# Kernel optimization log

Measured on AMD Instinct MI355X. Metric: run time of the kernel, lower is better.

The kernel has to match this reference:

```python
import jax, jax.numpy as jnp
import numpy as np

EPS = 1e-5  # torch LayerNorm default
H, DH = 8, 64  # heads, dim_head


def _ln(x, g, b):
    mu = jnp.mean(x, axis=-1, keepdims=True)
    var = jnp.var(x, axis=-1, keepdims=True)
    return (x - mu) / jnp.sqrt(var + EPS) * g + b


def setup_inputs() -> dict:
    key = jax.random.key(0)
    ks = jax.random.split(key, 8)
    B, N, M, D, CD = 4, 2048, 256, 1024, 768
    J = M + 1 + N  # context + null + self
    return {
        "x": jax.random.normal(ks[0], (B, N, D), jnp.float32),
        "context": jax.random.normal(ks[1], (B, M, CD), jnp.float32),
        "att_bias": jax.random.normal(ks[2], (B, H, N, J), jnp.float32) * 0.02,
        "ln_g": jnp.ones((D,), jnp.float32),
        "ln_b": jnp.zeros((D,), jnp.float32),
        "null_kv": jax.random.normal(ks[3], (2, DH), jnp.float32),
        "Wq": jax.random.normal(ks[4], (D, H * DH), jnp.float32) * 0.02,
        "Wkv": jax.random.normal(ks[5], (D, 2 * DH), jnp.float32) * 0.02,
        "cln_g": jnp.ones((CD,), jnp.float32),
        "cln_b": jnp.zeros((CD,), jnp.float32),
        "Wc": jax.random.normal(ks[6], (CD, 2 * DH), jnp.float32) * 0.02,
        "bc": jnp.zeros((2 * DH,), jnp.float32),
        "Wo": jax.random.normal(ks[7], (H * DH, D), jnp.float32) * 0.02,
        "oln_g": jnp.ones((D,), jnp.float32),
        "oln_b": jnp.zeros((D,), jnp.float32),
    }


def reference(x, context, att_bias, ln_g, ln_b, null_kv, Wq, Wkv,
              cln_g, cln_b, Wc, bc, Wo, oln_g, oln_b):
    B, N, D = x.shape
    scale = DH ** -0.5
    xn = _ln(x, ln_g, ln_b)
    # queries: per-head [b,h,n,dh], pre-scaled
    q = (xn @ Wq).reshape(B, N, H, DH).transpose(0, 2, 1, 3) * scale
    # shared single-head k/v [b,n,dh]
    kv = xn @ Wkv
    k, v = kv[..., :DH], kv[..., DH:]
    # context k/v [b,m,dh]
    ckv = _ln(context, cln_g, cln_b) @ Wc + bc
    ck, cv = ckv[..., :DH], ckv[..., DH:]
    # null kv token [b,1,dh]
    nk = jnp.broadcast_to(null_kv[0], (B, 1, DH))
    nv = jnp.broadcast_to(null_kv[1], (B, 1, DH))
    # torch order: cat null first, then context -> (ck, nk, k)
    k = jnp.concatenate([ck, nk, k], axis=1)  # [b, j, dh]
    v = jnp.concatenate([cv, nv, v], axis=1)
    score = jnp.einsum('bhid,bjd->bhij', q, k) + att_bias
    probs = jax.nn.softmax(score.astype(jnp.float32), axis=-1).astype(v.dtype)
    att = jnp.einsum('bhij,bjd->bhid', probs, v)
    att = att.transpose(0, 2, 1, 3).reshape(B, N, H * DH)
    return _ln(att @ Wo, oln_g, oln_b)
```

## Files before the change

### kernel.cpp

```cpp
#include <hip/hip_runtime.h>
#include <hip/hip_bf16.h>
#include <cstdint>
#include <cstddef>

#define Bq  4
#define Nq  2048
#define Mq  256
#define Dq  1024
#define CDq 768
#define Hq  8
#define DHq 64
#define Jq  2305
#define QKVN 640
#define NCH 37
#define J2  (NCH * 64)

typedef __bf16  bf16x8 __attribute__((ext_vector_type(8)));
typedef float   f32x4  __attribute__((ext_vector_type(4)));
typedef float   f32x4u __attribute__((ext_vector_type(4), aligned(4)));
typedef float   f32x16 __attribute__((ext_vector_type(16)));
typedef short   s16x8  __attribute__((ext_vector_type(8)));
typedef unsigned int u32x4 __attribute__((ext_vector_type(4)));
typedef unsigned short u16;
typedef unsigned int   u32;

__device__ __forceinline__ u16 f2b(float v) {
  unsigned x = __builtin_bit_cast(unsigned, v);
  unsigned r = (x + 0x7fffu + ((x >> 16) & 1u)) >> 16;
  return (u16)r;
}
__device__ __forceinline__ float b2f(u16 u) {
  unsigned x = ((unsigned)u) << 16;
  return __builtin_bit_cast(float, x);
}
__device__ __forceinline__ u32 cvtpk(float lo, float hi) {
  u32 r;
  asm("v_cvt_pk_bf16_f32 %0, %1, %2" : "=v"(r) : "v"(lo), "v"(hi));
  return r;
}
__device__ __forceinline__ void pswap(u32& a, u32& b) {
  asm volatile("v_permlane32_swap_b32 %0, %1" : "+v"(a), "+v"(b));
}
__device__ __forceinline__ f32x4 mfma16(bf16x8 a, bf16x8 b, f32x4 c) {
  return __builtin_amdgcn_mfma_f32_16x16x32_bf16(a, b, c, 0, 0, 0);
}
__device__ __forceinline__ f32x16 mfma32(bf16x8 a, bf16x8 b, f32x16 c) {
  return __builtin_amdgcn_mfma_f32_32x32x16_bf16(a, b, c, 0, 0, 0);
}
__device__ __forceinline__ bf16x8 frag_ld(const u16* p) {
  return __builtin_bit_cast(bf16x8, *(const s16x8*)p);
}
__device__ __forceinline__ void stout(float* p, float v) { *p = v; }
__device__ __forceinline__ void stout(u16*   p, float v) { *p = f2b(v); }

__device__ __forceinline__ void gl_lds16(const void* gSrc, void* ldsDst) {
  __builtin_amdgcn_global_load_lds(
      (const __attribute__((address_space(1))) void*)gSrc,
      (__attribute__((address_space(3))) void*)ldsDst, 16, 0, 0);
}

__global__ __launch_bounds__(256) void prep_kernel(
    const float* __restrict__ x,   const float* __restrict__ ln_g,
    const float* __restrict__ ln_b, u16* __restrict__ xn,
    const float* __restrict__ ctx, const float* __restrict__ cln_g,
    const float* __restrict__ cln_b, u16* __restrict__ ctxn,
    const float* __restrict__ Wq, const float* __restrict__ Wkv,
    const float* __restrict__ Wc, const float* __restrict__ Wo,
    u16* __restrict__ WqkvT, u16* __restrict__ WcT, u16* __restrict__ WoT) {
  const int tid = threadIdx.x;
  if (blockIdx.x < Bq * Nq + Bq * Mq) {
    const int row = blockIdx.x;
    const float* in; const float* g; const float* bb; u16* out; int D;
    if (row < Bq * Nq) {
      in = x + (size_t)row * Dq; g = ln_g; bb = ln_b;
      out = xn + (size_t)row * Dq; D = Dq;
    } else {
      int r2 = row - Bq * Nq;
      in = ctx + (size_t)r2 * CDq; g = cln_g; bb = cln_b;
      out = ctxn + (size_t)r2 * CDq; D = CDq;
    }
    __shared__ float buf[1024];
    __shared__ float red[8];
    float s = 0.f, s2 = 0.f;
    for (int i = tid; i < D; i += 256) {
      float v = in[i];
      buf[i] = v;
      s += v; s2 += v * v;
    }
    #pragma unroll
    for (int off = 32; off; off >>= 1) {
      s  += __shfl_down(s,  off);
      s2 += __shfl_down(s2, off);
    }
    if ((tid & 63) == 0) { red[tid >> 6] = s; red[4 + (tid >> 6)] = s2; }
    __syncthreads();
    float sum = red[0] + red[1] + red[2] + red[3];
    float sq  = red[4] + red[5] + red[6] + red[7];
    float mean = sum / D;
    float var  = sq / D - mean * mean;
    float rstd = rsqrtf(var + 1e-5f);
    for (int i = tid; i < D; i += 256)
      out[i] = f2b((buf[i] - mean) * rstd * g[i] + bb[i]);
  } else {
    __shared__ float T[32][33];
    int bid = blockIdx.x - (Bq * Nq + Bq * Mq);
    const float* W; u16* WT; int K, N, bx, by;
    if (bid < 512)      { W = Wq;  WT = WqkvT;                    K = 1024; N = 512;  bx = bid % 16;        by = bid / 16; }
    else if (bid < 640) { W = Wkv; WT = WqkvT + (size_t)512*1024; K = 1024; N = 128;  bx = (bid-512) % 4;   by = (bid-512) / 4; }
    else if (bid < 736) { W = Wc;  WT = WcT;                      K = 768;  N = 128;  bx = (bid-640) % 4;   by = (bid-640) / 4; }
    else                { W = Wo;  WT = WoT;                      K = 512;  N = 1024; bx = (bid-736) % 32;  by = (bid-736) / 32; }
    const int n0 = bx * 32, k0 = by * 32;
    const int tx = tid & 31, ty = tid >> 5;
    #pragma unroll
    for (int i = 0; i < 32; i += 8)
      T[ty + i][tx] = W[(size_t)(k0 + ty + i) * N + n0 + tx];
    __syncthreads();
    #pragma unroll
    for (int i = 0; i < 32; i += 8)
      WT[(size_t)(n0 + ty + i) * K + k0 + tx] = f2b(T[tx][ty + i]);
  }
}

__global__ __launch_bounds__(256) void ln_out_kernel(
    const float* __restrict__ in, const float* __restrict__ g,
    const float* __restrict__ bb, float* __restrict__ out) {
  const int row = blockIdx.x;
  const int tid = threadIdx.x;
  __shared__ float buf[1024];
  __shared__ float red[8];
  const float* xr = in + (size_t)row * Dq;
  float s = 0.f, s2 = 0.f;
  for (int i = tid; i < Dq; i += 256) {
    float v = xr[i];
    buf[i] = v;
    s += v; s2 += v * v;
  }
  #pragma unroll
  for (int off = 32; off; off >>= 1) {
    s  += __shfl_down(s,  off);
    s2 += __shfl_down(s2, off);
  }
  if ((tid & 63) == 0) { red[tid >> 6] = s; red[4 + (tid >> 6)] = s2; }
  __syncthreads();
  float sum = red[0] + red[1] + red[2] + red[3];
  float sq  = red[4] + red[5] + red[6] + red[7];
  float mean = sum / Dq;
  float var  = sq / Dq - mean * mean;
  float rstd = rsqrtf(var + 1e-5f);
  for (int i = tid; i < Dq; i += 256)
    out[(size_t)row * Dq + i] = (buf[i] - mean) * rstd * g[i] + bb[i];
}

template <typename OT>
__device__ __forceinline__ void gemm_body(const u16* __restrict__ A,
                                          const u16* __restrict__ BT,
                                          OT* __restrict__ C,
                                          int N, int K, int m0, int n0,
                                          u16* Al, u16* Bl) {
  const int tid  = threadIdx.x;
  const int lane = tid & 63, wave = tid >> 6;
  const int l16  = lane & 15, lhi = lane >> 4;
  const int wm = (wave >> 1) * 64, wn = (wave & 1) * 64;

  const int offB = (wave << 10) + (lane << 4);
  const int srow = offB >> 6;
  const int scby = offB & 63;

  f32x4 acc[4][4];
  #pragma unroll
  for (int i = 0; i < 4; ++i)
    #pragma unroll
    for (int j = 0; j < 4; ++j) acc[i][j] = f32x4{0.f, 0.f, 0.f, 0.f};

  for (int k0 = 0; k0 < K; k0 += 32) {
    __syncthreads();
    #pragma unroll
    for (int c = 0; c < 2; ++c) {
      gl_lds16((const char*)(A  + (size_t)(m0 + srow + c * 64) * K + k0) + scby,
               (char*)Al + c * 4096 + (wave << 10));
      gl_lds16((const char*)(BT + (size_t)(n0 + srow + c * 64) * K + k0) + scby,
               (char*)Bl + c * 4096 + (wave << 10));
    }
    __syncthreads();

    bf16x8 af[4], bfr[4];
    #pragma unroll
    for (int mt = 0; mt < 4; ++mt)
      af[mt] = frag_ld(Al + (wm + mt * 16 + l16) * 32 + lhi * 8);
    #pragma unroll
    for (int nt = 0; nt < 4; ++nt)
      bfr[nt] = frag_ld(Bl + (wn + nt * 16 + l16) * 32 + lhi * 8);
    __builtin_amdgcn_s_setprio(1);
    #pragma unroll
    for (int mt = 0; mt < 4; ++mt)
      #pragma unroll
      for (int nt = 0; nt < 4; ++nt)
        acc[mt][nt] = mfma16(af[mt], bfr[nt], acc[mt][nt]);
    __builtin_amdgcn_s_setprio(0);
  }

  #pragma unroll
  for (int mt = 0; mt < 4; ++mt)
    #pragma unroll
    for (int nt = 0; nt < 4; ++nt)
      #pragma unroll
      for (int r = 0; r < 4; ++r)
        stout(C + (size_t)(m0 + wm + mt * 16 + lhi * 4 + r) * N
                + (n0 + wn + nt * 16 + l16),
              acc[mt][nt][r]);
}

__global__ __launch_bounds__(256) void gemm_qkv_ckv(
    const u16* __restrict__ xn, const u16* __restrict__ WqkvT,
    u16* __restrict__ qkv,
    const u16* __restrict__ ctxn, const u16* __restrict__ WcT,
    u16* __restrict__ ckvb) {
  const u16 *A, *BT; u16* C; int N, K, m0, n0;
  if (blockIdx.y < 5) {
    A = xn; BT = WqkvT; C = qkv; N = QKVN; K = Dq;
    m0 = blockIdx.x * 128; n0 = blockIdx.y * 128;
  } else {
    if (blockIdx.x >= 8) return;
    A = ctxn; BT = WcT; C = ckvb; N = 2 * DHq; K = CDq;
    m0 = blockIdx.x * 128; n0 = 0;
  }
  __shared__ __align__(16) u16 Al[128 * 32];
  __shared__ __align__(16) u16 Bl[128 * 32];
  gemm_body<u16>(A, BT, C, N, K, m0, n0, Al, Bl);
}

__global__ __launch_bounds__(256) void gemm128f(const u16* __restrict__ A,
                                                const u16* __restrict__ BT,
                                                float* __restrict__ C,
                                                int N, int K) {
  __shared__ __align__(16) u16 Al[128 * 32];
  __shared__ __align__(16) u16 Bl[128 * 32];
  gemm_body<float>(A, BT, C, N, K, blockIdx.x * 128, blockIdx.y * 128, Al, Bl);
}

__global__ void build_kv(const u16* __restrict__ qkv,
                         const u16* __restrict__ ckvb,
                         const float* __restrict__ nullkv,
                         const float* __restrict__ bc,
                         u16* __restrict__ Kt, u16* __restrict__ Vt) {
  int idx = blockIdx.x * 256 + threadIdx.x;
  if (idx >= Bq * J2 * 64) return;
  int d = idx & 63;
  int t = idx >> 6;
  int j = t % J2;
  int b = t / J2;
  float k = 0.f, v = 0.f;
  if (j < Mq) {
    const u16* p = ckvb + (size_t)(b * Mq + j) * 128;
    k = b2f(p[d])      + bc[d];
    v = b2f(p[64 + d]) + bc[64 + d];
  } else if (j == Mq) {
    k = nullkv[d];
    v = nullkv[64 + d];
  } else if (j < Jq) {
    const u16* p = qkv + (size_t)(b * Nq + (j - Mq - 1)) * QKVN + 512;
    k = b2f(p[d]);
    v = b2f(p[64 + d]);
  }
  int ch = j >> 6, row = j & 63;
  char* tbase = (char*)Kt + ((size_t)(b * NCH + ch)) * 8192;
  *(u16*)(tbase + row * 128 + ((d << 1) ^ ((row & 7) << 4))) = f2b(k);
  char* vbase = (char*)Vt + ((size_t)(b * NCH + ch)) * 8192;
  *(u16*)(vbase + d * 128 + ((row << 1) ^ ((d & 7) << 4))) = f2b(v);
}

__global__ __launch_bounds__(128) void attn_kernel(
    const u16* __restrict__ qkv, const u16* __restrict__ Kt,
    const u16* __restrict__ Vt, const float* __restrict__ bias,
    u16* __restrict__ att) {
  __shared__ __align__(16) u16 Kl [2][4096];
  __shared__ __align__(16) u16 VTl[2][4096];
  const int tid  = threadIdx.x;
  const int wave = tid >> 6, lane = tid & 63;
  const int l = lane & 31, hi = lane >> 5;
  const int qt = blockIdx.x, h = blockIdx.y, b = blockIdx.z;
  const int qrow0 = qt * 64 + wave * 32;

  bf16x8 qf[4];
  {
    const u16* qp = qkv + ((size_t)(b * Nq + qrow0 + l)) * QKVN
                        + h * DHq + hi * 8;
    #pragma unroll
    for (int kt = 0; kt < 4; ++kt) qf[kt] = frag_ld(qp + kt * 16);
  }

  float m_s = -INFINITY, l_s = 0.f;
  f32x16 oacc[2];
  #pragma unroll
  for (int dt = 0; dt < 2; ++dt)
    #pragma unroll
    for (int r = 0; r < 16; ++r) oacc[dt][r] = 0.f;

  const float* bp = bias
      + ((size_t)((b * Hq + h) * (size_t)Nq + qrow0 + l)) * Jq + 4 * hi;

  const size_t tb0 = (size_t)b * NCH;
  const int soff = (wave << 12) + (lane << 4);

  auto stage = [&](int buf, int ch) {
    const char* kt_ = (const char*)Kt + (tb0 + ch) * 8192 + soff;
    const char* vt_ = (const char*)Vt + (tb0 + ch) * 8192 + soff;
    char* kl = (char*)&Kl[buf][0]  + (wave << 12);
    char* vl = (char*)&VTl[buf][0] + (wave << 12);
    #pragma unroll
    for (int i = 0; i < 4; ++i) {
      gl_lds16(kt_ + i * 1024, kl + i * 1024);
      gl_lds16(vt_ + i * 1024, vl + i * 1024);
    }
  };

  f32x4 bv[2][4];
  auto loadBias = [&](int ch) {
    const int jc = ch * 64;
    if (ch < NCH - 1) {
      #pragma unroll
      for (int jt = 0; jt < 2; ++jt)
        #pragma unroll
        for (int g = 0; g < 4; ++g)
          bv[jt][g] = (f32x4)(*(const f32x4u*)(bp + jc + jt * 32 + 8 * g));
    } else {
      #pragma unroll
      for (int jt = 0; jt < 2; ++jt)
        #pragma unroll
        for (int g = 0; g < 4; ++g)
          #pragma unroll
          for (int e = 0; e < 4; ++e) {
            int jg = jc + jt * 32 + 8 * g + 4 * hi + e;
            bv[jt][g][e] = (jg < Jq) ? bp[jc + jt * 32 + 8 * g + e] : -1e30f;
          }
    }
  };

  stage(0, 0);
  loadBias(0);
  __syncthreads();

  for (int ch = 0; ch < NCH; ++ch) {
    const int cur = ch & 1;
    if (ch + 1 < NCH) stage(cur ^ 1, ch + 1);
    const char* kbase = (const char*)&Kl[cur][0];
    const char* vbase = (const char*)&VTl[cur][0];

    f32x16 sacc[2];
    #pragma unroll
    for (int jt = 0; jt < 2; ++jt)
      #pragma unroll
      for (int r = 0; r < 16; ++r) sacc[jt][r] = 0.f;
    __builtin_amdgcn_s_setprio(1);
    #pragma unroll
    for (int jt = 0; jt < 2; ++jt) {
      const int row = jt * 32 + l;
      const int sw = (row & 7) << 4;
      #pragma unroll
      for (int kt = 0; kt < 4; ++kt) {
        bf16x8 kf = frag_ld((const u16*)(kbase + row * 128
                                         + ((kt * 32 + hi * 16) ^ sw)));
        sacc[jt] = mfma32(kf, qf[kt], sacc[jt]);
      }
    }
    __builtin_amdgcn_s_setprio(0);

    float sv[2][16];
    #pragma unroll
    for (int jt = 0; jt < 2; ++jt)
      #pragma unroll
      for (int r = 0; r < 16; ++r)
        sv[jt][r] = sacc[jt][r] * 0.125f + bv[jt][r >> 2][r & 3];
    if (ch + 1 < NCH) loadBias(ch + 1);

    float pmax = sv[0][0];
    #pragma unroll
    for (int jt = 0; jt < 2; ++jt)
      #pragma unroll
      for (int r = 0; r < 16; ++r) pmax = fmaxf(pmax, sv[jt][r]);
    pmax = fmaxf(pmax, __shfl_xor(pmax, 32));

    if (__any(pmax > m_s + 8.f)) {
      float mnew = fmaxf(m_s, pmax);
      float corr = __expf(m_s - mnew);
      l_s *= corr;
      m_s = mnew;
      #pragma unroll
      for (int r = 0; r < 16; ++r) {
        float c = __shfl(corr, (r & 3) + 8 * (r >> 2) + 4 * hi);
        oacc[0][r] *= c;
        oacc[1][r] *= c;
      }
    }

    float ps = 0.f;
    #pragma unroll
    for (int jt = 0; jt < 2; ++jt)
      #pragma unroll
      for (int r = 0; r < 16; ++r) {
        float pv = __expf(sv[jt][r] - m_s);
        sv[jt][r] = pv;
        ps += pv;
      }
    ps += __shfl_xor(ps, 32);
    l_s += ps;

    u32 pk[2][8];
    #pragma unroll
    for (int jt = 0; jt < 2; ++jt)
      #pragma unroll
      for (int g = 0; g < 4; ++g) {
        pk[jt][2 * g]     = cvtpk(sv[jt][4 * g],     sv[jt][4 * g + 1]);
        pk[jt][2 * g + 1] = cvtpk(sv[jt][4 * g + 2], sv[jt][4 * g + 3]);
      }

    #pragma unroll
    for (int kt = 0; kt < 4; ++kt) {
      const int t = kt & 1, js = kt >> 1;
      u32 a0 = pk[js][4 * t],     b0 = pk[js][4 * t + 2];
      u32 a1 = pk[js][4 * t + 1], b1 = pk[js][4 * t + 3];
      pswap(a0, b0);
      pswap(a1, b1);
      bf16x8 paf = __builtin_bit_cast(bf16x8, u32x4{a0, a1, b0, b1});
      __builtin_amdgcn_s_setprio(1);
      #pragma unroll
      for (int dt = 0; dt < 2; ++dt) {
        const int vrow = dt * 32 + l;
        bf16x8 vf = frag_ld((const u16*)(vbase + vrow * 128
                     + ((kt * 32 + hi * 16) ^ ((vrow & 7) << 4))));
        oacc[dt] = mfma32(paf, vf, oacc[dt]);
      }
      __builtin_amdgcn_s_setprio(0);
    }
    __syncthreads();
  }

  float linv = 1.0f / l_s;
  #pragma unroll
  for (int r = 0; r < 16; ++r) {
    const int qo = (r & 3) + 8 * (r >> 2) + 4 * hi;
    float inv = __shfl(linv, qo);
    u16* op = att + ((size_t)(b * Nq + qrow0 + qo)) * (Hq * DHq) + h * DHq + l;
    op[0]  = f2b(oacc[0][r] * inv);
    op[32] = f2b(oacc[1][r] * inv);
  }
}

extern "C" void kernel_launch(void* const* d_in, const int* in_sizes, int n_in,
                              void* d_out, int out_size, void* d_ws, size_t ws_size,
                              hipStream_t stream) {
  const float* x       = (const float*)d_in[0];
  const float* context = (const float*)d_in[1];
  const float* att_bias= (const float*)d_in[2];
  const float* ln_g    = (const float*)d_in[3];
  const float* ln_b    = (const float*)d_in[4];
  const float* null_kv = (const float*)d_in[5];
  const float* Wq      = (const float*)d_in[6];
  const float* Wkv     = (const float*)d_in[7];
  const float* cln_g   = (const float*)d_in[8];
  const float* cln_b   = (const float*)d_in[9];
  const float* Wc      = (const float*)d_in[10];
  const float* bc      = (const float*)d_in[11];
  const float* Wo      = (const float*)d_in[12];
  const float* oln_g   = (const float*)d_in[13];
  const float* oln_b   = (const float*)d_in[14];
  float* out = (float*)d_out;

  char* p = (char*)d_ws;
  auto alloc = [&](size_t bytes) {
    void* r = (void*)p;
    p += (bytes + 255) & ~(size_t)255;
    return r;
  };
  u16* xn     = (u16*)alloc((size_t)Bq * Nq * Dq * 2);
  u16* ctxn   = (u16*)alloc((size_t)Bq * Mq * CDq * 2);
  u16* WqkvT  = (u16*)alloc((size_t)QKVN * Dq * 2);
  u16* WcT    = (u16*)alloc((size_t)2 * DHq * CDq * 2);
  u16* WoT    = (u16*)alloc((size_t)Dq * Hq * DHq * 2);
  u16* qkv    = (u16*)alloc((size_t)Bq * Nq * QKVN * 2);
  u16* ckvb   = (u16*)alloc((size_t)Bq * Mq * 2 * DHq * 2);
  u16* Ktil   = (u16*)alloc((size_t)Bq * NCH * 8192);
  u16* Vtil   = (u16*)alloc((size_t)Bq * NCH * 8192);
  u16* attb   = (u16*)alloc((size_t)Bq * Nq * Hq * DHq * 2);
  float* y    = (float*)alloc((size_t)Bq * Nq * Dq * 4);

  prep_kernel<<<Bq * Nq + Bq * Mq + 1248, 256, 0, stream>>>(
      x, ln_g, ln_b, xn, context, cln_g, cln_b, ctxn,
      Wq, Wkv, Wc, Wo, WqkvT, WcT, WoT);

  gemm_qkv_ckv<<<dim3(Bq * Nq / 128, 6), 256, 0, stream>>>(
      xn, WqkvT, qkv, ctxn, WcT, ckvb);

  build_kv<<<(Bq * J2 * 64 + 255) / 256, 256, 0, stream>>>(
      qkv, ckvb, null_kv, bc, Ktil, Vtil);

  attn_kernel<<<dim3(Nq / 64, Hq, Bq), 128, 0, stream>>>(
      qkv, Ktil, Vtil, att_bias, attb);

  gemm128f<<<dim3(Bq * Nq / 128, Dq / 128), 256, 0, stream>>>(
      attb, WoT, y, Dq, Hq * DHq);
  ln_out_kernel<<<Bq * Nq, 256, 0, stream>>>(y, oln_g, oln_b, out);
}
```

Before: 261.7 us.

## Load K/V fragments directly from global memory, dropping LDS staging

The attention kernel no longer stages K and V chunks into double-buffered shared memory. Each wave now loads its MFMA fragments straight from global (L2-cached) memory into registers, and the XOR swizzle is removed from the repack kernel. Bias prefetch is reorganised into ping-pong register buffers with an unrolled two-step loop. This removes the LDS traffic and the per-chunk __syncthreads, but both waves of a block now fetch the same K/V data from global memory, which adds cache traffic and register pressure.

```diff
diff --git a/kernel.cpp b/kernel.cpp
--- a/kernel.cpp
+++ b/kernel.cpp
@@ -17,7 +17,6 @@
 
 typedef __bf16  bf16x8 __attribute__((ext_vector_type(8)));
 typedef float   f32x4  __attribute__((ext_vector_type(4)));
-typedef float   f32x4u __attribute__((ext_vector_type(4), aligned(4)));
 typedef float   f32x16 __attribute__((ext_vector_type(16)));
 typedef short   s16x8  __attribute__((ext_vector_type(8)));
 typedef unsigned int u32x4 __attribute__((ext_vector_type(4)));
@@ -264,17 +263,15 @@
   }
   int ch = j >> 6, row = j & 63;
   char* tbase = (char*)Kt + ((size_t)(b * NCH + ch)) * 8192;
-  *(u16*)(tbase + row * 128 + ((d << 1) ^ ((row & 7) << 4))) = f2b(k);
+  *(u16*)(tbase + row * 128 + (d << 1)) = f2b(k);
   char* vbase = (char*)Vt + ((size_t)(b * NCH + ch)) * 8192;
-  *(u16*)(vbase + d * 128 + ((row << 1) ^ ((d & 7) << 4))) = f2b(v);
+  *(u16*)(vbase + d * 128 + (row << 1)) = f2b(v);
 }
 
 __global__ __launch_bounds__(128) void attn_kernel(
     const u16* __restrict__ qkv, const u16* __restrict__ Kt,
     const u16* __restrict__ Vt, const float* __restrict__ bias,
     u16* __restrict__ att) {
-  __shared__ __align__(16) u16 Kl [2][4096];
-  __shared__ __align__(16) u16 VTl[2][4096];
   const int tid  = threadIdx.x;
   const int wave = tid >> 6, lane = tid & 63;
   const int l = lane & 31, hi = lane >> 5;
@@ -299,30 +296,17 @@
   const float* bp = bias
       + ((size_t)((b * Hq + h) * (size_t)Nq + qrow0 + l)) * Jq + 4 * hi;
 
-  const size_t tb0 = (size_t)b * NCH;
-  const int soff = (wave << 12) + (lane << 4);
-
-  auto stage = [&](int buf, int ch) {
-    const char* kt_ = (const char*)Kt + (tb0 + ch) * 8192 + soff;
-    const char* vt_ = (const char*)Vt + (tb0 + ch) * 8192 + soff;
-    char* kl = (char*)&Kl[buf][0]  + (wave << 12);
-    char* vl = (char*)&VTl[buf][0] + (wave << 12);
-    #pragma unroll
-    for (int i = 0; i < 4; ++i) {
-      gl_lds16(kt_ + i * 1024, kl + i * 1024);
-      gl_lds16(vt_ + i * 1024, vl + i * 1024);
-    }
-  };
-
-  f32x4 bv[2][4];
-  auto loadBias = [&](int ch) {
+  const char* kb0 = (const char*)Kt + (size_t)b * NCH * 8192 + l * 128 + hi * 16;
+  const char* vb0 = (const char*)Vt + (size_t)b * NCH * 8192 + l * 128 + hi * 16;
+
+  auto loadBias = [&](f32x4 (&bv)[2][4], int ch) {
     const int jc = ch * 64;
     if (ch < NCH - 1) {
       #pragma unroll
       for (int jt = 0; jt < 2; ++jt)
         #pragma unroll
         for (int g = 0; g < 4; ++g)
-          bv[jt][g] = (f32x4)(*(const f32x4u*)(bp + jc + jt * 32 + 8 * g));
+          bv[jt][g] = *(const f32x4*)(bp + jc + jt * 32 + 8 * g);
     } else {
       #pragma unroll
       for (int jt = 0; jt < 2; ++jt)
@@ -336,15 +320,25 @@
     }
   };
 
-  stage(0, 0);
-  loadBias(0);
-  __syncthreads();
-
-  for (int ch = 0; ch < NCH; ++ch) {
-    const int cur = ch & 1;
-    if (ch + 1 < NCH) stage(cur ^ 1, ch + 1);
-    const char* kbase = (const char*)&Kl[cur][0];
-    const char* vbase = (const char*)&VTl[cur][0];
+  f32x4 bvA[2][4], bvB[2][4];
+  loadBias(bvA, 0);
+
+  auto body = [&](int ch, f32x4 (&bvC)[2][4], f32x4 (&bvN)[2][4]) {
+    const char* kc = kb0 + (size_t)ch * 8192;
+    const char* vc = vb0 + (size_t)ch * 8192;
+
+    bf16x8 kf[8], vf[8];
+    #pragma unroll
+    for (int jt = 0; jt < 2; ++jt)
+      #pragma unroll
+      for (int kt = 0; kt < 4; ++kt)
+        kf[jt * 4 + kt] = frag_ld((const u16*)(kc + jt * 4096 + kt * 32));
+    #pragma unroll
+    for (int dt = 0; dt < 2; ++dt)
+      #pragma unroll
+      for (int kt = 0; kt < 4; ++kt)
+        vf[dt * 4 + kt] = frag_ld((const u16*)(vc + dt * 4096 + kt * 32));
+    if (ch + 1 < NCH) loadBias(bvN, ch + 1);
 
     f32x16 sacc[2];
     #pragma unroll
@@ -353,16 +347,10 @@
       for (int r = 0; r < 16; ++r) sacc[jt][r] = 0.f;
     __builtin_amdgcn_s_setprio(1);
     #pragma unroll
-    for (int jt = 0; jt < 2; ++jt) {
-      const int row = jt * 32 + l;
-      const int sw = (row & 7) << 4;
-      #pragma unroll
-      for (int kt = 0; kt < 4; ++kt) {
-        bf16x8 kf = frag_ld((const u16*)(kbase + row * 128
-                                         + ((kt * 32 + hi * 16) ^ sw)));
-        sacc[jt] = mfma32(kf, qf[kt], sacc[jt]);
-      }
-    }
+    for (int jt = 0; jt < 2; ++jt)
+      #pragma unroll
+      for (int kt = 0; kt < 4; ++kt)
+        sacc[jt] = mfma32(kf[jt * 4 + kt], qf[kt], sacc[jt]);
     __builtin_amdgcn_s_setprio(0);
 
     float sv[2][16];
@@ -370,8 +358,7 @@
     for (int jt = 0; jt < 2; ++jt)
       #pragma unroll
       for (int r = 0; r < 16; ++r)
-        sv[jt][r] = sacc[jt][r] * 0.125f + bv[jt][r >> 2][r & 3];
-    if (ch + 1 < NCH) loadBias(ch + 1);
+        sv[jt][r] = sacc[jt][r] * 0.125f + bvC[jt][r >> 2][r & 3];
 
     float pmax = sv[0][0];
     #pragma unroll
@@ -424,15 +411,18 @@
       bf16x8 paf = __builtin_bit_cast(bf16x8, u32x4{a0, a1, b0, b1});
       __builtin_amdgcn_s_setprio(1);
       #pragma unroll
-      for (int dt = 0; dt < 2; ++dt) {
-        const int vrow = dt * 32 + l;
-        bf16x8 vf = frag_ld((const u16*)(vbase + vrow * 128
-                     + ((kt * 32 + hi * 16) ^ ((vrow & 7) << 4))));
-        oacc[dt] = mfma32(paf, vf, oacc[dt]);
-      }
+      for (int dt = 0; dt < 2; ++dt)
+        oacc[dt] = mfma32(paf, vf[dt * 4 + kt], oacc[dt]);
       __builtin_amdgcn_s_setprio(0);
     }
-    __syncthreads();
+  };
+
+  int ch = 0;
+  while (true) {
+    body(ch, bvA, bvB);
+    if (++ch == NCH) break;
+    body(ch, bvB, bvA);
+    if (++ch == NCH) break;
   }
 
   float linv = 1.0f / l_s;
```

New measurement: 316.7 us. 1.21x slower.

## Prefetch attention bias two chunks ahead and store output GEMM in bf16

Applied to the files above, without the earlier changes.

The attention loop is unrolled four ways and rotates four bias register sets, so bias loads for chunks ch+2 and ch+3 are issued early. Barriers use partial vmcnt waits so outstanding bias loads can stay in flight across chunks, which targets the latency of the large att_bias stream. Separately, the output projection now writes bf16 instead of fp32, and the final LayerNorm reads bf16 with vector loads, halving the intermediate's traffic at some precision cost. The extra bias registers may raise register pressure in the attention kernel.

```diff
diff --git a/kernel.cpp b/kernel.cpp
--- a/kernel.cpp
+++ b/kernel.cpp
@@ -20,6 +20,7 @@
 typedef float   f32x4u __attribute__((ext_vector_type(4), aligned(4)));
 typedef float   f32x16 __attribute__((ext_vector_type(16)));
 typedef short   s16x8  __attribute__((ext_vector_type(8)));
+typedef short   s16x4  __attribute__((ext_vector_type(4)));
 typedef unsigned int u32x4 __attribute__((ext_vector_type(4)));
 typedef unsigned short u16;
 typedef unsigned int   u32;
@@ -122,18 +123,22 @@
 }
 
 __global__ __launch_bounds__(256) void ln_out_kernel(
-    const float* __restrict__ in, const float* __restrict__ g,
+    const u16* __restrict__ in, const float* __restrict__ g,
     const float* __restrict__ bb, float* __restrict__ out) {
   const int row = blockIdx.x;
   const int tid = threadIdx.x;
   __shared__ float buf[1024];
   __shared__ float red[8];
-  const float* xr = in + (size_t)row * Dq;
+  const u16* xr = in + (size_t)row * Dq;
   float s = 0.f, s2 = 0.f;
-  for (int i = tid; i < Dq; i += 256) {
-    float v = xr[i];
-    buf[i] = v;
-    s += v; s2 += v * v;
+  {
+    s16x4 v4 = *(const s16x4*)(xr + tid * 4);
+    #pragma unroll
+    for (int e = 0; e < 4; ++e) {
+      float v = b2f((u16)v4[e]);
+      buf[tid * 4 + e] = v;
+      s += v; s2 += v * v;
+    }
   }
   #pragma unroll
   for (int off = 32; off; off >>= 1) {
@@ -147,8 +152,11 @@
   float mean = sum / Dq;
   float var  = sq / Dq - mean * mean;
   float rstd = rsqrtf(var + 1e-5f);
-  for (int i = tid; i < Dq; i += 256)
+  #pragma unroll
+  for (int e = 0; e < 4; ++e) {
+    int i = tid * 4 + e;
     out[(size_t)row * Dq + i] = (buf[i] - mean) * rstd * g[i] + bb[i];
+  }
 }
 
 template <typename OT>
@@ -229,13 +237,13 @@
   gemm_body<u16>(A, BT, C, N, K, m0, n0, Al, Bl);
 }
 
-__global__ __launch_bounds__(256) void gemm128f(const u16* __restrict__ A,
+__global__ __launch_bounds__(256) void gemm128b(const u16* __restrict__ A,
                                                 const u16* __restrict__ BT,
-                                                float* __restrict__ C,
+                                                u16* __restrict__ C,
                                                 int N, int K) {
   __shared__ __align__(16) u16 Al[128 * 32];
   __shared__ __align__(16) u16 Bl[128 * 32];
-  gemm_body<float>(A, BT, C, N, K, blockIdx.x * 128, blockIdx.y * 128, Al, Bl);
+  gemm_body<u16>(A, BT, C, N, K, blockIdx.x * 128, blockIdx.y * 128, Al, Bl);
 }
 
 __global__ void build_kv(const u16* __restrict__ qkv,
@@ -314,8 +322,7 @@
     }
   };
 
-  f32x4 bv[2][4];
-  auto loadBias = [&](int ch) {
+  auto loadBias = [&](f32x4 (&bv)[2][4], int ch) {
     const int jc = ch * 64;
     if (ch < NCH - 1) {
       #pragma unroll
@@ -336,13 +343,8 @@
     }
   };
 
-  stage(0, 0);
-  loadBias(0);
-  __syncthreads();
-
-  for (int ch = 0; ch < NCH; ++ch) {
+  auto compute = [&](int ch, f32x4 (&bvC)[2][4]) {
     const int cur = ch & 1;
-    if (ch + 1 < NCH) stage(cur ^ 1, ch + 1);
     const char* kbase = (const char*)&Kl[cur][0];
     const char* vbase = (const char*)&VTl[cur][0];
 
@@ -365,19 +367,17 @@
     }
     __builtin_amdgcn_s_setprio(0);
 
-    float sv[2][16];
     #pragma unroll
     for (int jt = 0; jt < 2; ++jt)
       #pragma unroll
       for (int r = 0; r < 16; ++r)
-        sv[jt][r] = sacc[jt][r] * 0.125f + bv[jt][r >> 2][r & 3];
-    if (ch + 1 < NCH) loadBias(ch + 1);
-
-    float pmax = sv[0][0];
+        sacc[jt][r] = sacc[jt][r] * 0.125f + bvC[jt][r >> 2][r & 3];
+
+    float pmax = sacc[0][0];
     #pragma unroll
     for (int jt = 0; jt < 2; ++jt)
       #pragma unroll
-      for (int r = 0; r < 16; ++r) pmax = fmaxf(pmax, sv[jt][r]);
+      for (int r = 0; r < 16; ++r) pmax = fmaxf(pmax, sacc[jt][r]);
     pmax = fmaxf(pmax, __shfl_xor(pmax, 32));
 
     if (__any(pmax > m_s + 8.f)) {
@@ -398,8 +398,8 @@
     for (int jt = 0; jt < 2; ++jt)
       #pragma unroll
       for (int r = 0; r < 16; ++r) {
-        float pv = __expf(sv[jt][r] - m_s);
-        sv[jt][r] = pv;
+        float pv = __expf(sacc[jt][r] - m_s);
+        sacc[jt][r] = pv;
         ps += pv;
       }
     ps += __shfl_xor(ps, 32);
@@ -410,8 +410,8 @@
     for (int jt = 0; jt < 2; ++jt)
       #pragma unroll
       for (int g = 0; g < 4; ++g) {
-        pk[jt][2 * g]     = cvtpk(sv[jt][4 * g],     sv[jt][4 * g + 1]);
-        pk[jt][2 * g + 1] = cvtpk(sv[jt][4 * g + 2], sv[jt][4 * g + 3]);
+        pk[jt][2 * g]     = cvtpk(sacc[jt][4 * g],     sacc[jt][4 * g + 1]);
+        pk[jt][2 * g + 1] = cvtpk(sacc[jt][4 * g + 2], sacc[jt][4 * g + 3]);
       }
 
     #pragma unroll
@@ -432,7 +432,57 @@
       }
       __builtin_amdgcn_s_setprio(0);
     }
-    __syncthreads();
+  };
+
+  auto barKeep = [&]() {
+    asm volatile("s_waitcnt vmcnt(16)" ::: "memory");
+    __builtin_amdgcn_s_barrier();
+    __builtin_amdgcn_sched_barrier(0);
+  };
+  auto barDrain = [&]() {
+    asm volatile("s_waitcnt vmcnt(0)" ::: "memory");
+    __builtin_amdgcn_s_barrier();
+    __builtin_amdgcn_sched_barrier(0);
+  };
+
+  f32x4 bv0[2][4], bv1[2][4], bv2[2][4], bv3[2][4];
+  stage(0, 0);
+  loadBias(bv0, 0);
+  loadBias(bv1, 1);
+  barKeep();
+
+  int ch = 0;
+  while (true) {
+    {
+      if (ch + 1 < NCH) stage((ch & 1) ^ 1, ch + 1);
+      const bool full = (ch + 3 < NCH);
+      if (ch + 2 < NCH) loadBias(bv2, ch + 2);
+      if (ch + 3 < NCH) loadBias(bv3, ch + 3);
+      compute(ch, bv0);
+      if (ch + 1 < NCH) { if (full) barKeep(); else barDrain(); }
+    }
+    if (++ch == NCH) break;
+    {
+      if (ch + 1 < NCH) stage((ch & 1) ^ 1, ch + 1);
+      compute(ch, bv1);
+      if (ch + 1 < NCH) barDrain();
+    }
+    if (++ch == NCH) break;
+    {
+      if (ch + 1 < NCH) stage((ch & 1) ^ 1, ch + 1);
+      const bool full = (ch + 3 < NCH);
+      if (ch + 2 < NCH) loadBias(bv0, ch + 2);
+      if (ch + 3 < NCH) loadBias(bv1, ch + 3);
+      compute(ch, bv2);
+      if (ch + 1 < NCH) { if (full) barKeep(); else barDrain(); }
+    }
+    if (++ch == NCH) break;
+    {
+      if (ch + 1 < NCH) stage((ch & 1) ^ 1, ch + 1);
+      compute(ch, bv3);
+      if (ch + 1 < NCH) barDrain();
+    }
+    if (++ch == NCH) break;
   }
 
   float linv = 1.0f / l_s;
@@ -482,7 +532,7 @@
   u16* Ktil   = (u16*)alloc((size_t)Bq * NCH * 8192);
   u16* Vtil   = (u16*)alloc((size_t)Bq * NCH * 8192);
   u16* attb   = (u16*)alloc((size_t)Bq * Nq * Hq * DHq * 2);
-  float* y    = (float*)alloc((size_t)Bq * Nq * Dq * 4);
+  u16* y      = (u16*)alloc((size_t)Bq * Nq * Dq * 2);
 
   prep_kernel<<<Bq * Nq + Bq * Mq + 1248, 256, 0, stream>>>(
       x, ln_g, ln_b, xn, context, cln_g, cln_b, ctxn,
@@ -497,7 +547,7 @@
   attn_kernel<<<dim3(Nq / 64, Hq, Bq), 128, 0, stream>>>(
       qkv, Ktil, Vtil, att_bias, attb);
 
-  gemm128f<<<dim3(Bq * Nq / 128, Dq / 128), 256, 0, stream>>>(
+  gemm128b<<<dim3(Bq * Nq / 128, Dq / 128), 256, 0, stream>>>(
       attb, WoT, y, Dq, Hq * DHq);
   ln_out_kernel<<<Bq * Nq, 256, 0, stream>>>(y, oln_g, oln_b, out);
 }
```

After: 275.4 us. 1.05x slower.

## Give each attention wave private K/V buffers and store out-proj result as bf16

Applied to the files above, without the earlier changes.

The attention kernel now gives each wave its own double-buffered copy of the K/V tiles. This removes the block-wide __syncthreads per chunk and replaces it with an explicit vmcnt wait, with bias prefetch ping-ponged between two register sets. Shared memory doubles and every wave loads the full tile redundantly. Separately, the output projection GEMM now writes bf16 instead of fp32, and the final LayerNorm reads bf16 vectors. This halves that intermediate's traffic at a small precision cost before normalization.

```diff
diff --git a/kernel.cpp b/kernel.cpp
--- a/kernel.cpp
+++ b/kernel.cpp
@@ -20,6 +20,7 @@
 typedef float   f32x4u __attribute__((ext_vector_type(4), aligned(4)));
 typedef float   f32x16 __attribute__((ext_vector_type(16)));
 typedef short   s16x8  __attribute__((ext_vector_type(8)));
+typedef short   s16x4  __attribute__((ext_vector_type(4)));
 typedef unsigned int u32x4 __attribute__((ext_vector_type(4)));
 typedef unsigned short u16;
 typedef unsigned int   u32;
@@ -122,18 +123,22 @@
 }
 
 __global__ __launch_bounds__(256) void ln_out_kernel(
-    const float* __restrict__ in, const float* __restrict__ g,
+    const u16* __restrict__ in, const float* __restrict__ g,
     const float* __restrict__ bb, float* __restrict__ out) {
   const int row = blockIdx.x;
   const int tid = threadIdx.x;
   __shared__ float buf[1024];
   __shared__ float red[8];
-  const float* xr = in + (size_t)row * Dq;
+  const u16* xr = in + (size_t)row * Dq;
   float s = 0.f, s2 = 0.f;
-  for (int i = tid; i < Dq; i += 256) {
-    float v = xr[i];
-    buf[i] = v;
-    s += v; s2 += v * v;
+  {
+    s16x4 v4 = *(const s16x4*)(xr + tid * 4);
+    #pragma unroll
+    for (int e = 0; e < 4; ++e) {
+      float v = b2f((u16)v4[e]);
+      buf[tid * 4 + e] = v;
+      s += v; s2 += v * v;
+    }
   }
   #pragma unroll
   for (int off = 32; off; off >>= 1) {
@@ -147,8 +152,11 @@
   float mean = sum / Dq;
   float var  = sq / Dq - mean * mean;
   float rstd = rsqrtf(var + 1e-5f);
-  for (int i = tid; i < Dq; i += 256)
+  #pragma unroll
+  for (int e = 0; e < 4; ++e) {
+    int i = tid * 4 + e;
     out[(size_t)row * Dq + i] = (buf[i] - mean) * rstd * g[i] + bb[i];
+  }
 }
 
 template <typename OT>
@@ -229,13 +237,13 @@
   gemm_body<u16>(A, BT, C, N, K, m0, n0, Al, Bl);
 }
 
-__global__ __launch_bounds__(256) void gemm128f(const u16* __restrict__ A,
+__global__ __launch_bounds__(256) void gemm128b(const u16* __restrict__ A,
                                                 const u16* __restrict__ BT,
-                                                float* __restrict__ C,
+                                                u16* __restrict__ C,
                                                 int N, int K) {
   __shared__ __align__(16) u16 Al[128 * 32];
   __shared__ __align__(16) u16 Bl[128 * 32];
-  gemm_body<float>(A, BT, C, N, K, blockIdx.x * 128, blockIdx.y * 128, Al, Bl);
+  gemm_body<u16>(A, BT, C, N, K, blockIdx.x * 128, blockIdx.y * 128, Al, Bl);
 }
 
 __global__ void build_kv(const u16* __restrict__ qkv,
@@ -273,8 +281,8 @@
     const u16* __restrict__ qkv, const u16* __restrict__ Kt,
     const u16* __restrict__ Vt, const float* __restrict__ bias,
     u16* __restrict__ att) {
-  __shared__ __align__(16) u16 Kl [2][4096];
-  __shared__ __align__(16) u16 VTl[2][4096];
+  __shared__ __align__(16) u16 Kl [2][2][4096];
+  __shared__ __align__(16) u16 VTl[2][2][4096];
   const int tid  = threadIdx.x;
   const int wave = tid >> 6, lane = tid & 63;
   const int l = lane & 31, hi = lane >> 5;
@@ -300,22 +308,21 @@
       + ((size_t)((b * Hq + h) * (size_t)Nq + qrow0 + l)) * Jq + 4 * hi;
 
   const size_t tb0 = (size_t)b * NCH;
-  const int soff = (wave << 12) + (lane << 4);
+  const int soff = lane << 4;
 
   auto stage = [&](int buf, int ch) {
     const char* kt_ = (const char*)Kt + (tb0 + ch) * 8192 + soff;
     const char* vt_ = (const char*)Vt + (tb0 + ch) * 8192 + soff;
-    char* kl = (char*)&Kl[buf][0]  + (wave << 12);
-    char* vl = (char*)&VTl[buf][0] + (wave << 12);
-    #pragma unroll
-    for (int i = 0; i < 4; ++i) {
+    char* kl = (char*)&Kl[wave][buf][0];
+    char* vl = (char*)&VTl[wave][buf][0];
+    #pragma unroll
+    for (int i = 0; i < 8; ++i) {
       gl_lds16(kt_ + i * 1024, kl + i * 1024);
       gl_lds16(vt_ + i * 1024, vl + i * 1024);
     }
   };
 
-  f32x4 bv[2][4];
-  auto loadBias = [&](int ch) {
+  auto loadBias = [&](f32x4 (&bv)[2][4], int ch) {
     const int jc = ch * 64;
     if (ch < NCH - 1) {
       #pragma unroll
@@ -336,15 +343,23 @@
     }
   };
 
+  f32x4 bvA[2][4], bvB[2][4];
   stage(0, 0);
-  loadBias(0);
-  __syncthreads();
-
-  for (int ch = 0; ch < NCH; ++ch) {
+  loadBias(bvA, 0);
+
+  auto body = [&](int ch, f32x4 (&bvC)[2][4], f32x4 (&bvN)[2][4]) {
     const int cur = ch & 1;
-    if (ch + 1 < NCH) stage(cur ^ 1, ch + 1);
-    const char* kbase = (const char*)&Kl[cur][0];
-    const char* vbase = (const char*)&VTl[cur][0];
+    if (ch + 1 < NCH) {
+      stage(cur ^ 1, ch + 1);
+      loadBias(bvN, ch + 1);
+      asm volatile("s_waitcnt vmcnt(24)" ::: "memory");
+    } else {
+      asm volatile("s_waitcnt vmcnt(0)" ::: "memory");
+    }
+    __builtin_amdgcn_sched_barrier(0);
+
+    const char* kbase = (const char*)&Kl[wave][cur][0];
+    const char* vbase = (const char*)&VTl[wave][cur][0];
 
     f32x16 sacc[2];
     #pragma unroll
@@ -370,8 +385,7 @@
     for (int jt = 0; jt < 2; ++jt)
       #pragma unroll
       for (int r = 0; r < 16; ++r)
-        sv[jt][r] = sacc[jt][r] * 0.125f + bv[jt][r >> 2][r & 3];
-    if (ch + 1 < NCH) loadBias(ch + 1);
+        sv[jt][r] = sacc[jt][r] * 0.125f + bvC[jt][r >> 2][r & 3];
 
     float pmax = sv[0][0];
     #pragma unroll
@@ -432,7 +446,14 @@
       }
       __builtin_amdgcn_s_setprio(0);
     }
-    __syncthreads();
+  };
+
+  int ch = 0;
+  while (true) {
+    body(ch, bvA, bvB);
+    if (++ch == NCH) break;
+    body(ch, bvB, bvA);
+    if (++ch == NCH) break;
   }
 
   float linv = 1.0f / l_s;
@@ -482,7 +503,7 @@
   u16* Ktil   = (u16*)alloc((size_t)Bq * NCH * 8192);
   u16* Vtil   = (u16*)alloc((size_t)Bq * NCH * 8192);
   u16* attb   = (u16*)alloc((size_t)Bq * Nq * Hq * DHq * 2);
-  float* y    = (float*)alloc((size_t)Bq * Nq * Dq * 4);
+  u16* y      = (u16*)alloc((size_t)Bq * Nq * Dq * 2);
 
   prep_kernel<<<Bq * Nq + Bq * Mq + 1248, 256, 0, stream>>>(
       x, ln_g, ln_b, xn, context, cln_g, cln_b, ctxn,
@@ -497,7 +518,7 @@
   attn_kernel<<<dim3(Nq / 64, Hq, Bq), 128, 0, stream>>>(
       qkv, Ktil, Vtil, att_bias, attb);
 
-  gemm128f<<<dim3(Bq * Nq / 128, Dq / 128), 256, 0, stream>>>(
+  gemm128b<<<dim3(Bq * Nq / 128, Dq / 128), 256, 0, stream>>>(
       attb, WoT, y, Dq, Hq * DHq);
   ln_out_kernel<<<Bq * Nq, 256, 0, stream>>>(y, oln_g, oln_b, out);
 }
```

New measurement: 290.2 us. 10.9% more time.
